# Kernel optimization log

Measured on AMD Instinct MI355X. Metric: run time of the kernel, lower is better.

The kernel has to match this reference:

```python
import jax, jax.numpy as jnp
import numpy as np


def _binarize_act(z):
    # STE: forward = sign(z), backward = d/dz clamp(z,-1,1)
    clipped = jnp.clip(z, -1.0, 1.0)
    return jax.lax.stop_gradient(jnp.sign(z) - clipped) + clipped


def _binarize_weight(w):
    # per-output-channel scaling factor = mean |w| over (in, kh, kw), detached
    scale = jax.lax.stop_gradient(jnp.mean(jnp.abs(w), axis=(1, 2, 3), keepdims=True))
    clipped = jnp.clip(w, -1.0, 1.0)
    return jax.lax.stop_gradient(scale * jnp.sign(w) - clipped) + clipped


def setup_inputs() -> dict:
    key = jax.random.key(0)
    k = jax.random.split(key, 6)
    B, C, H, W = 16, 64, 256, 256
    return {
        "x": jax.random.normal(k[0], (B, C, H, W), dtype=jnp.float32),
        "move0_bias": jax.random.normal(k[1], (1, C, 1, 1), dtype=jnp.float32) * 0.1,
        "conv_weight": jax.random.normal(k[2], (C, C, 3, 3), dtype=jnp.float32) * 0.1,
        "prelu_weight": jnp.full((C,), 0.25, dtype=jnp.float32)
        + jax.random.normal(k[3], (C,), dtype=jnp.float32) * 0.01,
        "pr_bias0": jax.random.normal(k[4], (1, C, 1, 1), dtype=jnp.float32) * 0.1,
        "pr_bias1": jax.random.normal(k[5], (1, C, 1, 1), dtype=jnp.float32) * 0.1,
    }


def reference(x, move0_bias, conv_weight, prelu_weight, pr_bias0, pr_bias1):
    identity = x  # stride=1, out_channels == in_channels -> no downsample / concat
    z = _binarize_act(x + move0_bias)
    bw = _binarize_weight(conv_weight)
    y = jax.lax.conv_general_dilated(
        z, bw, window_strides=(1, 1), padding=((1, 1), (1, 1)),
        dimension_numbers=("NCHW", "OIHW", "NCHW"))
    # RPReLU: bias0 -> per-channel PReLU -> bias1
    y = y + pr_bias0
    a = prelu_weight.reshape(1, -1, 1, 1)
    y = jnp.where(y > 0, y, a * y)
    y = y + pr_bias1
    return y + identity
```

## Files before the change

kernel.cpp:

```cpp
#include <hip/hip_runtime.h>
#include <stdint.h>

#define Bn 16
#define C 64
#define H 256
#define W 256
#define HW (H * W)
#define NHW (Bn * HW)

#define TW 64
#define TH 16
#define SZH 18
#define SZW 73

typedef float f32x4 __attribute__((ext_vector_type(4)));
typedef float f32x2 __attribute__((ext_vector_type(2)));

__global__ void prep_weights(const float* __restrict__ w,
                             uint64_t* __restrict__ wbits,
                             float* __restrict__ scale,
                             int* __restrict__ edgeL,
                             int* __restrict__ edgeR) {
    int o = blockIdx.x;
    int c = threadIdx.x;
    const float* wp = w + ((size_t)o * C + c) * 9;
    float asum = 0.f;
    uint64_t m[9];
#pragma unroll
    for (int tap = 0; tap < 9; ++tap) {
        float v = wp[tap];
        asum += fabsf(v);
        m[tap] = __ballot(v > 0.f);
    }
    if (c == 0) {
#pragma unroll
        for (int tap = 0; tap < 9; ++tap) wbits[o * 9 + tap] = m[tap];
        edgeL[o] = 2 * (int)(__popcll(m[0]) + __popcll(m[3]) + __popcll(m[6]));
        edgeR[o] = 2 * (int)(__popcll(m[2]) + __popcll(m[5]) + __popcll(m[8]));
    }
#pragma unroll
    for (int off = 32; off > 0; off >>= 1)
        asum += __shfl_down(asum, off);
    if (c == 0) scale[o] = asum * (1.f / 576.f);
}

__global__ __launch_bounds__(512, 8) void bconv_fused(
        const uint64_t* __restrict__ wbits,
        const float* __restrict__ scale,
        const int* __restrict__ edgeL,
        const int* __restrict__ edgeR,
        const float* __restrict__ x,
        const float* __restrict__ bias,
        const float* __restrict__ pb0,
        const float* __restrict__ aw,
        const float* __restrict__ pb1,
        float* __restrict__ out) {
    __shared__ uint64_t sz[SZH * SZW];

    int t = threadIdx.x;
    int bid = blockIdx.x;
    int n = bid >> 6;
    int tile = bid & 63;
    int ty = tile >> 2, tx = tile & 3;
    int gh0 = ty * TH, gw0 = tx * TW;

    const float* xn = x + (size_t)n * C * HW;

    if (t < SZH * 18) {
        int r = t / 18;
        int cb = (t - r * 18) * 4;
        int gh = gh0 + r - 1;
        int gwb = gw0 - 4 + cb;
        uint64_t b0 = 0, b1 = 0, b2 = 0, b3 = 0;
        if ((unsigned)gh < (unsigned)H && (unsigned)gwb <= (unsigned)(W - 4)) {
            const float* xp = xn + gh * W + gwb;
#pragma unroll 8
            for (int ch = 0; ch < C; ++ch) {
                f32x4 v = *reinterpret_cast<const f32x4*>(xp + (size_t)ch * HW);
                float bc = bias[ch];
                b0 |= (uint64_t)(v.x + bc > 0.f) << ch;
                b1 |= (uint64_t)(v.y + bc > 0.f) << ch;
                b2 |= (uint64_t)(v.z + bc > 0.f) << ch;
                b3 |= (uint64_t)(v.w + bc > 0.f) << ch;
            }
        }
        uint64_t* zp = &sz[r * SZW + cb];
        zp[0] = b0; zp[1] = b1; zp[2] = b2; zp[3] = b3;
    }
    __syncthreads();

    int tr = t >> 5;
    int tc2 = (t & 31) * 2;
    int gh = gh0 + tr;
    int gw = gw0 + tc2;

    uint64_t zb[3][4];
#pragma unroll
    for (int i = 0; i < 3; ++i)
#pragma unroll
        for (int j = 0; j < 4; ++j)
            zb[i][j] = sz[(tr + i) * SZW + tc2 + 3 + j];

    const float* xid = xn + gh * W + gw;
    float* op = out + (size_t)n * C * HW + gh * W + gw;
    bool leftE  = (gw == 0);
    bool rightE = (gw == W - 2);

    bool slowW = (ty == 0 && tr < 2) || (ty == 15 && tr >= 14);

    if (!slowW) {
        f32x2 id0 = *reinterpret_cast<const f32x2*>(xid);
        f32x2 id1 = *reinterpret_cast<const f32x2*>(xid + HW);
#pragma unroll 2
        for (int o = 0; o < C; ++o) {
            const uint64_t* wp = wbits + o * 9;
            int s0 = 0, s1 = 0;
#pragma unroll
            for (int i = 0; i < 3; ++i)
#pragma unroll
                for (int jj = 0; jj < 3; ++jj) {
                    uint64_t wt = wp[i * 3 + jj];
                    s0 += (int)__popcll(wt ^ zb[i][jj]);
                    s1 += (int)__popcll(wt ^ zb[i][jj + 1]);
                }
            int d0 = 576 - 2 * s0, d1 = 576 - 2 * s1;
            if (leftE)  d0 += edgeL[o] - 192;
            if (rightE) d1 += edgeR[o] - 192;

            float sc = scale[o], bb0 = pb0[o], af = aw[o], bb1 = pb1[o];
            f32x2 idv = id0;
            id0 = id1;
            if (o < C - 2)
                id1 = *reinterpret_cast<const f32x2*>(xid + (size_t)(o + 2) * HW);
            f32x2 r;
            float y;
            y = sc * (float)d0 + bb0; y = y > 0.f ? y : af * y; r.x = y + bb1 + idv.x;
            y = sc * (float)d1 + bb0; y = y > 0.f ? y : af * y; r.y = y + bb1 + idv.y;
            __builtin_nontemporal_store(r, reinterpret_cast<f32x2*>(op + (size_t)o * HW));
        }
    } else {
        int vrow[3], vcol[4];
#pragma unroll
        for (int i = 0; i < 3; ++i)
            vrow[i] = ((unsigned)(gh - 1 + i) < (unsigned)H) ? -1 : 0;
#pragma unroll
        for (int j = 0; j < 4; ++j)
            vcol[j] = ((unsigned)(gw - 1 + j) < (unsigned)W) ? -1 : 0;
        int nr  = (vrow[0] & 1) + (vrow[1] & 1) + (vrow[2] & 1);
        int nv0 = nr * ((vcol[0] & 1) + (vcol[1] & 1) + (vcol[2] & 1));
        int nv1 = nr * ((vcol[1] & 1) + (vcol[2] & 1) + (vcol[3] & 1));
#pragma unroll 2
        for (int o = 0; o < C; ++o) {
            const uint64_t* wp = wbits + o * 9;
            int s0 = 0, s1 = 0;
#pragma unroll
            for (int i = 0; i < 3; ++i)
#pragma unroll
                for (int jj = 0; jj < 3; ++jj) {
                    uint64_t wt = wp[i * 3 + jj];
                    s0 += (vrow[i] & vcol[jj])     & (int)__popcll(wt ^ zb[i][jj]);
                    s1 += (vrow[i] & vcol[jj + 1]) & (int)__popcll(wt ^ zb[i][jj + 1]);
                }
            float sc = scale[o], bb0 = pb0[o], af = aw[o], bb1 = pb1[o];
            f32x2 idv = *reinterpret_cast<const f32x2*>(xid + (size_t)o * HW);
            f32x2 r;
            float y;
            y = sc * (float)(64 * nv0 - 2 * s0) + bb0; y = y > 0.f ? y : af * y; r.x = y + bb1 + idv.x;
            y = sc * (float)(64 * nv1 - 2 * s1) + bb0; y = y > 0.f ? y : af * y; r.y = y + bb1 + idv.y;
            __builtin_nontemporal_store(r, reinterpret_cast<f32x2*>(op + (size_t)o * HW));
        }
    }
}

extern "C" void kernel_launch(void* const* d_in, const int* in_sizes, int n_in,
                              void* d_out, int out_size, void* d_ws, size_t ws_size,
                              hipStream_t stream) {
    const float* x           = (const float*)d_in[0];
    const float* move0_bias  = (const float*)d_in[1];
    const float* conv_weight = (const float*)d_in[2];
    const float* prelu_w     = (const float*)d_in[3];
    const float* pr_bias0    = (const float*)d_in[4];
    const float* pr_bias1    = (const float*)d_in[5];
    float* out = (float*)d_out;

    uint8_t* ws = (uint8_t*)d_ws;
    uint64_t* wbits = (uint64_t*)ws;
    float* scale    = (float*)(ws + 4608);
    int* edgeL      = (int*)(ws + 4864);
    int* edgeR      = (int*)(ws + 5120);

    prep_weights<<<64, 64, 0, stream>>>(conv_weight, wbits, scale, edgeL, edgeR);
    bconv_fused<<<Bn * (H / TH) * (W / TW), 512, 0, stream>>>(
        wbits, scale, edgeL, edgeR, x, move0_bias,
        pr_bias0, prelu_w, pr_bias1, out);
}
```

Measured before the change: 559.9 us.

## Pack per-channel params, pad weight bits, deepen identity prefetch in binary conv

Packs scale, bias0, PReLU slope and bias1 into one float4 per output channel and the edge corrections into an int2, so each channel needs fewer scalar loads. Pads each channel's weight bitmask row to 10 words for aligned access. Unrolls the output-channel loop by 4 with the identity residual loaded four channels ahead, and relaxes launch bounds from 8 to 4 waves per SIMD so the extra prefetch has register room. This hides more global load latency, at the cost of higher register use and possibly lower occupancy.

```diff
diff --git a/kernel.cpp b/kernel.cpp
--- a/kernel.cpp
+++ b/kernel.cpp
@@ -17,10 +17,12 @@
 typedef float f32x2 __attribute__((ext_vector_type(2)));
 
 __global__ void prep_weights(const float* __restrict__ w,
-                             uint64_t* __restrict__ wbits,
-                             float* __restrict__ scale,
-                             int* __restrict__ edgeL,
-                             int* __restrict__ edgeR) {
+                             const float* __restrict__ pb0,
+                             const float* __restrict__ aw,
+                             const float* __restrict__ pb1,
+                             uint64_t* __restrict__ wbitsP,
+                             float4* __restrict__ prm,
+                             int2* __restrict__ edg) {
     int o = blockIdx.x;
     int c = threadIdx.x;
     const float* wp = w + ((size_t)o * C + c) * 9;
@@ -34,26 +36,24 @@
     }
     if (c == 0) {
 #pragma unroll
-        for (int tap = 0; tap < 9; ++tap) wbits[o * 9 + tap] = m[tap];
-        edgeL[o] = 2 * (int)(__popcll(m[0]) + __popcll(m[3]) + __popcll(m[6]));
-        edgeR[o] = 2 * (int)(__popcll(m[2]) + __popcll(m[5]) + __popcll(m[8]));
+        for (int tap = 0; tap < 9; ++tap) wbitsP[o * 10 + tap] = m[tap];
+        wbitsP[o * 10 + 9] = 0;
+        edg[o] = make_int2(
+            2 * (int)(__popcll(m[0]) + __popcll(m[3]) + __popcll(m[6])) - 192,
+            2 * (int)(__popcll(m[2]) + __popcll(m[5]) + __popcll(m[8])) - 192);
     }
 #pragma unroll
     for (int off = 32; off > 0; off >>= 1)
         asum += __shfl_down(asum, off);
-    if (c == 0) scale[o] = asum * (1.f / 576.f);
+    if (c == 0) prm[o] = make_float4(asum * (1.f / 576.f), pb0[o], aw[o], pb1[o]);
 }
 
-__global__ __launch_bounds__(512, 8) void bconv_fused(
-        const uint64_t* __restrict__ wbits,
-        const float* __restrict__ scale,
-        const int* __restrict__ edgeL,
-        const int* __restrict__ edgeR,
+__global__ __launch_bounds__(512, 4) void bconv_fused(
+        const uint64_t* __restrict__ wbitsP,
+        const float4* __restrict__ prm,
+        const int2* __restrict__ edg,
         const float* __restrict__ x,
         const float* __restrict__ bias,
-        const float* __restrict__ pb0,
-        const float* __restrict__ aw,
-        const float* __restrict__ pb1,
         float* __restrict__ out) {
     __shared__ uint64_t sz[SZH * SZW];
 
@@ -74,7 +74,7 @@
         uint64_t b0 = 0, b1 = 0, b2 = 0, b3 = 0;
         if ((unsigned)gh < (unsigned)H && (unsigned)gwb <= (unsigned)(W - 4)) {
             const float* xp = xn + gh * W + gwb;
-#pragma unroll 8
+#pragma unroll 16
             for (int ch = 0; ch < C; ++ch) {
                 f32x4 v = *reinterpret_cast<const f32x4*>(xp + (size_t)ch * HW);
                 float bc = bias[ch];
@@ -108,35 +108,48 @@
 
     bool slowW = (ty == 0 && tr < 2) || (ty == 15 && tr >= 14);
 
+    auto proc = [&](int oc, f32x2 iv) {
+        const uint64_t* wp = wbitsP + oc * 10;
+        int s0 = 0, s1 = 0;
+#pragma unroll
+        for (int i = 0; i < 3; ++i)
+#pragma unroll
+            for (int jj = 0; jj < 3; ++jj) {
+                uint64_t wt = wp[i * 3 + jj];
+                s0 += (int)__popcll(wt ^ zb[i][jj]);
+                s1 += (int)__popcll(wt ^ zb[i][jj + 1]);
+            }
+        int d0 = 576 - 2 * s0, d1 = 576 - 2 * s1;
+        int2 e = edg[oc];
+        if (leftE)  d0 += e.x;
+        if (rightE) d1 += e.y;
+        float4 pr = prm[oc];
+        f32x2 r;
+        float y;
+        y = pr.x * (float)d0 + pr.y; y = y > 0.f ? y : pr.z * y; r.x = y + pr.w + iv.x;
+        y = pr.x * (float)d1 + pr.y; y = y > 0.f ? y : pr.z * y; r.y = y + pr.w + iv.y;
+        __builtin_nontemporal_store(r, reinterpret_cast<f32x2*>(op + (size_t)oc * HW));
+    };
+
     if (!slowW) {
         f32x2 id0 = *reinterpret_cast<const f32x2*>(xid);
-        f32x2 id1 = *reinterpret_cast<const f32x2*>(xid + HW);
-#pragma unroll 2
-        for (int o = 0; o < C; ++o) {
-            const uint64_t* wp = wbits + o * 9;
-            int s0 = 0, s1 = 0;
-#pragma unroll
-            for (int i = 0; i < 3; ++i)
-#pragma unroll
-                for (int jj = 0; jj < 3; ++jj) {
-                    uint64_t wt = wp[i * 3 + jj];
-                    s0 += (int)__popcll(wt ^ zb[i][jj]);
-                    s1 += (int)__popcll(wt ^ zb[i][jj + 1]);
-                }
-            int d0 = 576 - 2 * s0, d1 = 576 - 2 * s1;
-            if (leftE)  d0 += edgeL[o] - 192;
-            if (rightE) d1 += edgeR[o] - 192;
-
-            float sc = scale[o], bb0 = pb0[o], af = aw[o], bb1 = pb1[o];
-            f32x2 idv = id0;
-            id0 = id1;
-            if (o < C - 2)
-                id1 = *reinterpret_cast<const f32x2*>(xid + (size_t)(o + 2) * HW);
-            f32x2 r;
-            float y;
-            y = sc * (float)d0 + bb0; y = y > 0.f ? y : af * y; r.x = y + bb1 + idv.x;
-            y = sc * (float)d1 + bb0; y = y > 0.f ? y : af * y; r.y = y + bb1 + idv.y;
-            __builtin_nontemporal_store(r, reinterpret_cast<f32x2*>(op + (size_t)o * HW));
+        f32x2 id1 = *reinterpret_cast<const f32x2*>(xid + (size_t)1 * HW);
+        f32x2 id2 = *reinterpret_cast<const f32x2*>(xid + (size_t)2 * HW);
+        f32x2 id3 = *reinterpret_cast<const f32x2*>(xid + (size_t)3 * HW);
+        for (int o = 0; o < C; o += 4) {
+            int p0 = o + 4 > C - 1 ? C - 1 : o + 4;
+            int p1 = o + 5 > C - 1 ? C - 1 : o + 5;
+            int p2 = o + 6 > C - 1 ? C - 1 : o + 6;
+            int p3 = o + 7 > C - 1 ? C - 1 : o + 7;
+            f32x2 n0 = *reinterpret_cast<const f32x2*>(xid + (size_t)p0 * HW);
+            f32x2 n1 = *reinterpret_cast<const f32x2*>(xid + (size_t)p1 * HW);
+            f32x2 n2 = *reinterpret_cast<const f32x2*>(xid + (size_t)p2 * HW);
+            f32x2 n3 = *reinterpret_cast<const f32x2*>(xid + (size_t)p3 * HW);
+            proc(o + 0, id0);
+            proc(o + 1, id1);
+            proc(o + 2, id2);
+            proc(o + 3, id3);
+            id0 = n0; id1 = n1; id2 = n2; id3 = n3;
         }
     } else {
         int vrow[3], vcol[4];
@@ -151,7 +164,7 @@
         int nv1 = nr * ((vcol[1] & 1) + (vcol[2] & 1) + (vcol[3] & 1));
 #pragma unroll 2
         for (int o = 0; o < C; ++o) {
-            const uint64_t* wp = wbits + o * 9;
+            const uint64_t* wp = wbitsP + o * 10;
             int s0 = 0, s1 = 0;
 #pragma unroll
             for (int i = 0; i < 3; ++i)
@@ -161,12 +174,12 @@
                     s0 += (vrow[i] & vcol[jj])     & (int)__popcll(wt ^ zb[i][jj]);
                     s1 += (vrow[i] & vcol[jj + 1]) & (int)__popcll(wt ^ zb[i][jj + 1]);
                 }
-            float sc = scale[o], bb0 = pb0[o], af = aw[o], bb1 = pb1[o];
+            float4 pr = prm[o];
             f32x2 idv = *reinterpret_cast<const f32x2*>(xid + (size_t)o * HW);
             f32x2 r;
             float y;
-            y = sc * (float)(64 * nv0 - 2 * s0) + bb0; y = y > 0.f ? y : af * y; r.x = y + bb1 + idv.x;
-            y = sc * (float)(64 * nv1 - 2 * s1) + bb0; y = y > 0.f ? y : af * y; r.y = y + bb1 + idv.y;
+            y = pr.x * (float)(64 * nv0 - 2 * s0) + pr.y; y = y > 0.f ? y : pr.z * y; r.x = y + pr.w + idv.x;
+            y = pr.x * (float)(64 * nv1 - 2 * s1) + pr.y; y = y > 0.f ? y : pr.z * y; r.y = y + pr.w + idv.y;
             __builtin_nontemporal_store(r, reinterpret_cast<f32x2*>(op + (size_t)o * HW));
         }
     }
@@ -184,13 +197,12 @@
     float* out = (float*)d_out;
 
     uint8_t* ws = (uint8_t*)d_ws;
-    uint64_t* wbits = (uint64_t*)ws;
-    float* scale    = (float*)(ws + 4608);
-    int* edgeL      = (int*)(ws + 4864);
-    int* edgeR      = (int*)(ws + 5120);
-
-    prep_weights<<<64, 64, 0, stream>>>(conv_weight, wbits, scale, edgeL, edgeR);
+    uint64_t* wbitsP = (uint64_t*)ws;
+    float4* prm      = (float4*)(ws + 5120);
+    int2* edg        = (int2*)(ws + 6144);
+
+    prep_weights<<<64, 64, 0, stream>>>(conv_weight, pr_bias0, prelu_w, pr_bias1,
+                                        wbitsP, prm, edg);
     bconv_fused<<<Bn * (H / TH) * (W / TW), 512, 0, stream>>>(
-        wbits, scale, edgeL, edgeR, x, move0_bias,
-        pr_bias0, prelu_w, pr_bias1, out);
+        wbitsP, prm, edg, x, move0_bias, out);
 }
```

Result: faster. 518.8 us (-7.3%).
